# Kernel optimization log

Measured on AMD Instinct MI355X. Metric: run time of the kernel, lower is better.

## Reference

```python
import jax, jax.numpy as jnp
import numpy as np


def setup_inputs() -> dict:
    key = jax.random.key(0)
    k1, k2 = jax.random.split(key)
    X = jax.random.normal(k1, (8192, 3), dtype=jnp.float32)
    Y = jax.random.normal(k2, (8192, 3), dtype=jnp.float32)
    return {"X": X, "Y": Y}


def reference(X, Y):
    # Pairwise L2 distances: torch.norm(x - y) for every (x, y) pair.
    # d[i, j] = ||X[i] - Y[j]||_2, shape [N, M]
    diff = X[:, None, :] - Y[None, :, :]          # [N, M, D]
    d = jnp.sqrt(jnp.sum(diff * diff, axis=-1))   # [N, M]
    hd_xy = jnp.max(jnp.min(d, axis=1))           # max over x of min over y
    hd_yx = jnp.max(jnp.min(d, axis=0))           # max over y of min over x
    return jnp.maximum(hd_xy, hd_yx)
```

## Files before the change

kernel.cpp:

```cpp
#include <hip/hip_runtime.h>
#include <math.h>


typedef float v2f __attribute__((ext_vector_type(2)));

constexpr int NPTS = 8192;
constexpr int T = 256;
constexpr int R = 4;
constexpr int ROWS_PB = T * R;
constexpr int RG = NPTS / ROWS_PB;
constexpr int CG = 64;
constexpr int COLS = NPTS / CG;

__global__ __launch_bounds__(T) void pair_partial_kernel(
        const float* __restrict__ X, const float* __restrict__ Y,
        float* __restrict__ partial, float* __restrict__ out) {
    int b = blockIdx.x;
    if (b == 0 && threadIdx.x == 0) out[0] = 0.f;
    int dir = b / (RG * CG);
    int rem = b - dir * (RG * CG);
    int rg = rem / CG;
    int cg = rem - rg * CG;
    const float* A = dir ? Y : X;
    const float* B = dir ? X : Y;

    int t = threadIdx.x;
    int r0 = rg * ROWS_PB + t;

    float ax[R], ay[R], az[R];
#pragma unroll
    for (int k = 0; k < R; ++k) {
        int row = r0 + k * T;
        ax[k] = A[row * 3 + 0];
        ay[k] = A[row * 3 + 1];
        az[k] = A[row * 3 + 2];
    }

    __shared__ float4 Bs[COLS];
    for (int i = t; i < COLS; i += T) {
        int j = cg * COLS + i;
        float bx = B[j * 3 + 0], by = B[j * 3 + 1], bz = B[j * 3 + 2];
        Bs[i] = make_float4(bx, by, bz, -0.5f * fmaf(bx, bx, fmaf(by, by, bz * bz)));
    }

    v2f ax2[R / 2], ay2[R / 2], az2[R / 2], na2[R / 2], mt2[R / 2];
#pragma unroll
    for (int q = 0; q < R / 2; ++q) {
        ax2[q] = (v2f){ax[2 * q], ax[2 * q + 1]};
        ay2[q] = (v2f){ay[2 * q], ay[2 * q + 1]};
        az2[q] = (v2f){az[2 * q], az[2 * q + 1]};
        na2[q] = ax2[q] * ax2[q] + ay2[q] * ay2[q] + az2[q] * az2[q];
        mt2[q] = (v2f){-__builtin_inff(), -__builtin_inff()};
    }
    __syncthreads();

#pragma unroll 4
    for (int j = 0; j < COLS; ++j) {
        float4 p = Bs[j];
        v2f px = (v2f){p.x, p.x};
        v2f py = (v2f){p.y, p.y};
        v2f pz = (v2f){p.z, p.z};
        v2f pw = (v2f){p.w, p.w};
#pragma unroll
        for (int q = 0; q < R / 2; ++q) {
            v2f tt = az2[q] * pz + pw;
            tt = ay2[q] * py + tt;
            tt = ax2[q] * px + tt;
            mt2[q].x = fmaxf(mt2[q].x, tt.x);
            mt2[q].y = fmaxf(mt2[q].y, tt.y);
        }
    }

    float* op = partial + (size_t)(dir * CG + cg) * NPTS + rg * ROWS_PB + t;
#pragma unroll
    for (int q = 0; q < R / 2; ++q) {
        op[(2 * q) * T]     = fmaf(-2.f, mt2[q].x, na2[q].x);
        op[(2 * q + 1) * T] = fmaf(-2.f, mt2[q].y, na2[q].y);
    }
}

__global__ __launch_bounds__(T) void reduce_final_kernel(
        const float* __restrict__ partial, float* __restrict__ out) {
    int rid = blockIdx.x * T + threadIdx.x;
    int dir = rid >> 13;
    int row = rid & (NPTS - 1);
    const float* p = partial + (size_t)dir * CG * NPTS + row;

    float m[8];
#pragma unroll
    for (int k = 0; k < 8; ++k) m[k] = __builtin_inff();
#pragma unroll
    for (int cg = 0; cg < CG; ++cg)
        m[cg & 7] = fminf(m[cg & 7], p[(size_t)cg * NPTS]);
#pragma unroll
    for (int k = 0; k < 4; ++k) m[k] = fminf(m[k], m[k + 4]);
    float mm = fminf(fminf(m[0], m[1]), fminf(m[2], m[3]));
    float d = sqrtf(fmaxf(mm, 0.f));

    for (int o = 32; o > 0; o >>= 1) d = fmaxf(d, __shfl_down(d, o));
    __shared__ float wm[T / 64];
    if ((threadIdx.x & 63) == 0) wm[threadIdx.x >> 6] = d;
    __syncthreads();
    if (threadIdx.x == 0) {
        float bm = wm[0];
        for (int w = 1; w < T / 64; ++w) bm = fmaxf(bm, wm[w]);
        atomicMax((unsigned*)out, __float_as_uint(bm));
    }
}


constexpr int SEG_J = 512;
constexpr int SEGS = NPTS / SEG_J;

__global__ void init_min_kernel(unsigned* wsmin, int n) {
    int i = blockIdx.x * blockDim.x + threadIdx.x;
    if (i < n) wsmin[i] = 0x7F800000u;
}

__global__ __launch_bounds__(T) void pair_min_kernel(
        const float* __restrict__ X, const float* __restrict__ Y,
        unsigned* __restrict__ minXY, unsigned* __restrict__ minYX) {
    constexpr int RPB = T * 8;
    constexpr int BLOCKS_PER_DIR = (NPTS / RPB) * SEGS;
    int b = blockIdx.x;
    int dir = b / BLOCKS_PER_DIR;
    int rem = b - dir * BLOCKS_PER_DIR;
    int rg = rem / SEGS;
    int seg = rem - rg * SEGS;
    const float* A = dir ? Y : X;
    const float* B = dir ? X : Y;
    unsigned* omin = dir ? minYX : minXY;

    __shared__ float Bs[SEG_J * 3];
    int t = threadIdx.x;
    const float* Bseg = B + seg * SEG_J * 3;
    for (int i = t; i < SEG_J * 3; i += T) Bs[i] = Bseg[i];

    int r0 = rg * RPB + t;
    float ax[8], ay[8], az[8], m[8];
#pragma unroll
    for (int r = 0; r < 8; ++r) {
        int row = r0 + r * T;
        ax[r] = A[row * 3 + 0];
        ay[r] = A[row * 3 + 1];
        az[r] = A[row * 3 + 2];
        m[r] = __builtin_inff();
    }
    __syncthreads();

#pragma unroll 2
    for (int j = 0; j < SEG_J; ++j) {
        float bx = Bs[3 * j + 0], by = Bs[3 * j + 1], bz = Bs[3 * j + 2];
#pragma unroll
        for (int r = 0; r < 8; ++r) {
            float dx = ax[r] - bx, dy = ay[r] - by, dz = az[r] - bz;
            m[r] = fminf(m[r], fmaf(dx, dx, fmaf(dy, dy, dz * dz)));
        }
    }
#pragma unroll
    for (int r = 0; r < 8; ++r)
        atomicMin(&omin[r0 + r * T], __float_as_uint(m[r]));
}

__global__ __launch_bounds__(T) void finalize_min_kernel(
        const unsigned* __restrict__ wsmin, float* __restrict__ out, int n) {
    int t = threadIdx.x;
    float mx = 0.f;
    for (int i = t; i < n; i += T) mx = fmaxf(mx, __uint_as_float(wsmin[i]));
    for (int o = 32; o > 0; o >>= 1) mx = fmaxf(mx, __shfl_down(mx, o));
    __shared__ float wmax[T / 64];
    if ((t & 63) == 0) wmax[t >> 6] = mx;
    __syncthreads();
    if (t == 0) {
        float mm = wmax[0];
        for (int w = 1; w < T / 64; ++w) mm = fmaxf(mm, wmax[w]);
        out[0] = sqrtf(mm);
    }
}

extern "C" void kernel_launch(void* const* d_in, const int* in_sizes, int n_in,
                              void* d_out, int out_size, void* d_ws, size_t ws_size,
                              hipStream_t stream) {
    const float* X = (const float*)d_in[0];
    const float* Y = (const float*)d_in[1];
    float* out = (float*)d_out;

    const size_t need = (size_t)(2 * CG * NPTS) * sizeof(float);

    if (ws_size >= need) {
        float* partial = (float*)d_ws;
        pair_partial_kernel<<<2 * RG * CG, T, 0, stream>>>(X, Y, partial, out);
        reduce_final_kernel<<<2 * NPTS / T, T, 0, stream>>>(partial, out);
    } else if (ws_size >= 2 * NPTS * sizeof(unsigned)) {
        unsigned* wsmin = (unsigned*)d_ws;
        init_min_kernel<<<(2 * NPTS + T - 1) / T, T, 0, stream>>>(wsmin, 2 * NPTS);
        pair_min_kernel<<<2 * (NPTS / (T * 8)) * SEGS, T, 0, stream>>>(
            X, Y, wsmin, wsmin + NPTS);
        finalize_min_kernel<<<1, T, 0, stream>>>(wsmin, out, 2 * NPTS);
    }
}
```

Before: 29.78 us.

## Halve column groups and finish reduction with last-block atomic counter

```diff
diff --git a/kernel.cpp b/kernel.cpp
--- a/kernel.cpp
+++ b/kernel.cpp
@@ -9,14 +9,17 @@
 constexpr int R = 4;
 constexpr int ROWS_PB = T * R;
 constexpr int RG = NPTS / ROWS_PB;
-constexpr int CG = 64;
+constexpr int CG = 32;
 constexpr int COLS = NPTS / CG;
+
+constexpr int RT = 64;
+constexpr int RBLK = 2 * NPTS / RT;
 
 __global__ __launch_bounds__(T) void pair_partial_kernel(
         const float* __restrict__ X, const float* __restrict__ Y,
-        float* __restrict__ partial, float* __restrict__ out) {
+        float* __restrict__ partial, unsigned* __restrict__ counter) {
     int b = blockIdx.x;
-    if (b == 0 && threadIdx.x == 0) out[0] = 0.f;
+    if (b == 0 && threadIdx.x == 0) *counter = 0u;
     int dir = b / (RG * CG);
     int rem = b - dir * (RG * CG);
     int rg = rem / CG;
@@ -27,13 +30,14 @@
     int t = threadIdx.x;
     int r0 = rg * ROWS_PB + t;
 
-    float ax[R], ay[R], az[R];
-#pragma unroll
-    for (int k = 0; k < R; ++k) {
-        int row = r0 + k * T;
-        ax[k] = A[row * 3 + 0];
-        ay[k] = A[row * 3 + 1];
-        az[k] = A[row * 3 + 2];
+    v2f ax2[R / 2], ay2[R / 2], az2[R / 2], na2[R / 2], mt2[R / 2];
+#pragma unroll
+    for (int q = 0; q < R / 2; ++q) {
+        int ra = r0 + (2 * q) * T;
+        int rb = r0 + (2 * q + 1) * T;
+        ax2[q] = (v2f){A[ra * 3 + 0], A[rb * 3 + 0]};
+        ay2[q] = (v2f){A[ra * 3 + 1], A[rb * 3 + 1]};
+        az2[q] = (v2f){A[ra * 3 + 2], A[rb * 3 + 2]};
     }
 
     __shared__ float4 Bs[COLS];
@@ -43,18 +47,14 @@
         Bs[i] = make_float4(bx, by, bz, -0.5f * fmaf(bx, bx, fmaf(by, by, bz * bz)));
     }
 
-    v2f ax2[R / 2], ay2[R / 2], az2[R / 2], na2[R / 2], mt2[R / 2];
 #pragma unroll
     for (int q = 0; q < R / 2; ++q) {
-        ax2[q] = (v2f){ax[2 * q], ax[2 * q + 1]};
-        ay2[q] = (v2f){ay[2 * q], ay[2 * q + 1]};
-        az2[q] = (v2f){az[2 * q], az[2 * q + 1]};
         na2[q] = ax2[q] * ax2[q] + ay2[q] * ay2[q] + az2[q] * az2[q];
         mt2[q] = (v2f){-__builtin_inff(), -__builtin_inff()};
     }
     __syncthreads();
 
-#pragma unroll 4
+#pragma unroll 8
     for (int j = 0; j < COLS; ++j) {
         float4 p = Bs[j];
         v2f px = (v2f){p.x, p.x};
@@ -66,8 +66,7 @@
             v2f tt = az2[q] * pz + pw;
             tt = ay2[q] * py + tt;
             tt = ax2[q] * px + tt;
-            mt2[q].x = fmaxf(mt2[q].x, tt.x);
-            mt2[q].y = fmaxf(mt2[q].y, tt.y);
+            mt2[q] = __builtin_elementwise_max(mt2[q], tt);
         }
     }
 
@@ -79,9 +78,10 @@
     }
 }
 
-__global__ __launch_bounds__(T) void reduce_final_kernel(
-        const float* __restrict__ partial, float* __restrict__ out) {
-    int rid = blockIdx.x * T + threadIdx.x;
+__global__ __launch_bounds__(RT) void reduce_final_kernel(
+        const float* __restrict__ partial, float* __restrict__ blockmax,
+        unsigned* __restrict__ counter, float* __restrict__ out) {
+    int rid = blockIdx.x * RT + threadIdx.x;
     int dir = rid >> 13;
     int row = rid & (NPTS - 1);
     const float* p = partial + (size_t)dir * CG * NPTS + row;
@@ -94,34 +94,46 @@
         m[cg & 7] = fminf(m[cg & 7], p[(size_t)cg * NPTS]);
 #pragma unroll
     for (int k = 0; k < 4; ++k) m[k] = fminf(m[k], m[k + 4]);
-    float mm = fminf(fminf(m[0], m[1]), fminf(m[2], m[3]));
-    float d = sqrtf(fmaxf(mm, 0.f));
-
-    for (int o = 32; o > 0; o >>= 1) d = fmaxf(d, __shfl_down(d, o));
-    __shared__ float wm[T / 64];
-    if ((threadIdx.x & 63) == 0) wm[threadIdx.x >> 6] = d;
-    __syncthreads();
-    if (threadIdx.x == 0) {
-        float bm = wm[0];
-        for (int w = 1; w < T / 64; ++w) bm = fmaxf(bm, wm[w]);
-        atomicMax((unsigned*)out, __float_as_uint(bm));
-    }
-}
-
-
-constexpr int SEG_J = 512;
-constexpr int SEGS = NPTS / SEG_J;
+    float mm = fmaxf(fminf(fminf(m[0], m[1]), fminf(m[2], m[3])), 0.f);
+
+#pragma unroll
+    for (int o = 32; o > 0; o >>= 1) mm = fmaxf(mm, __shfl_xor(mm, o));
+    if (threadIdx.x == 0)
+        __hip_atomic_store(&blockmax[blockIdx.x], mm, __ATOMIC_RELEASE,
+                           __HIP_MEMORY_SCOPE_AGENT);
+
+    __shared__ unsigned is_last;
+    if (threadIdx.x == 0)
+        is_last = (__hip_atomic_fetch_add(counter, 1u, __ATOMIC_ACQ_REL,
+                                          __HIP_MEMORY_SCOPE_AGENT) == RBLK - 1);
+    __syncthreads();
+    if (!is_last) return;
+
+    float bm = 0.f;
+#pragma unroll
+    for (int k = 0; k < RBLK / RT; ++k) {
+        float v = __hip_atomic_load(&blockmax[k * RT + threadIdx.x],
+                                    __ATOMIC_ACQUIRE, __HIP_MEMORY_SCOPE_AGENT);
+        bm = fmaxf(bm, v);
+    }
+#pragma unroll
+    for (int o = 32; o > 0; o >>= 1) bm = fmaxf(bm, __shfl_xor(bm, o));
+    if (threadIdx.x == 0) out[0] = sqrtf(bm);
+}
+
 
 __global__ void init_min_kernel(unsigned* wsmin, int n) {
     int i = blockIdx.x * blockDim.x + threadIdx.x;
     if (i < n) wsmin[i] = 0x7F800000u;
 }
 
-__global__ __launch_bounds__(T) void pair_min_kernel(
+__global__ __launch_bounds__(256) void pair_min_kernel(
         const float* __restrict__ X, const float* __restrict__ Y,
         unsigned* __restrict__ minXY, unsigned* __restrict__ minYX) {
-    constexpr int RPB = T * 8;
-    constexpr int BLOCKS_PER_DIR = (NPTS / RPB) * SEGS;
+    constexpr int SEG_J = 512;
+    constexpr int SEGS = NPTS / SEG_J;
+    constexpr int RPB8 = 256 * 8;
+    constexpr int BLOCKS_PER_DIR = (NPTS / RPB8) * SEGS;
     int b = blockIdx.x;
     int dir = b / BLOCKS_PER_DIR;
     int rem = b - dir * BLOCKS_PER_DIR;
@@ -134,13 +146,13 @@
     __shared__ float Bs[SEG_J * 3];
     int t = threadIdx.x;
     const float* Bseg = B + seg * SEG_J * 3;
-    for (int i = t; i < SEG_J * 3; i += T) Bs[i] = Bseg[i];
-
-    int r0 = rg * RPB + t;
+    for (int i = t; i < SEG_J * 3; i += 256) Bs[i] = Bseg[i];
+
+    int r0 = rg * RPB8 + t;
     float ax[8], ay[8], az[8], m[8];
 #pragma unroll
     for (int r = 0; r < 8; ++r) {
-        int row = r0 + r * T;
+        int row = r0 + r * 256;
         ax[r] = A[row * 3 + 0];
         ay[r] = A[row * 3 + 1];
         az[r] = A[row * 3 + 2];
@@ -159,21 +171,20 @@
     }
 #pragma unroll
     for (int r = 0; r < 8; ++r)
-        atomicMin(&omin[r0 + r * T], __float_as_uint(m[r]));
-}
-
-__global__ __launch_bounds__(T) void finalize_min_kernel(
+        atomicMin(&omin[r0 + r * 256], __float_as_uint(m[r]));
+}
+
+__global__ __launch_bounds__(256) void finalize_min_kernel(
         const unsigned* __restrict__ wsmin, float* __restrict__ out, int n) {
     int t = threadIdx.x;
     float mx = 0.f;
-    for (int i = t; i < n; i += T) mx = fmaxf(mx, __uint_as_float(wsmin[i]));
+    for (int i = t; i < n; i += 256) mx = fmaxf(mx, __uint_as_float(wsmin[i]));
     for (int o = 32; o > 0; o >>= 1) mx = fmaxf(mx, __shfl_down(mx, o));
-    __shared__ float wmax[T / 64];
+    __shared__ float wmax[4];
     if ((t & 63) == 0) wmax[t >> 6] = mx;
     __syncthreads();
     if (t == 0) {
-        float mm = wmax[0];
-        for (int w = 1; w < T / 64; ++w) mm = fmaxf(mm, wmax[w]);
+        float mm = fmaxf(fmaxf(wmax[0], wmax[1]), fmaxf(wmax[2], wmax[3]));
         out[0] = sqrtf(mm);
     }
 }
@@ -185,17 +196,20 @@
     const float* Y = (const float*)d_in[1];
     float* out = (float*)d_out;
 
-    const size_t need = (size_t)(2 * CG * NPTS) * sizeof(float);
+    const size_t partial_elems = (size_t)2 * CG * NPTS;
+    const size_t need = (partial_elems + RBLK + 1) * sizeof(float);
 
     if (ws_size >= need) {
         float* partial = (float*)d_ws;
-        pair_partial_kernel<<<2 * RG * CG, T, 0, stream>>>(X, Y, partial, out);
-        reduce_final_kernel<<<2 * NPTS / T, T, 0, stream>>>(partial, out);
+        float* blockmax = partial + partial_elems;
+        unsigned* counter = (unsigned*)(blockmax + RBLK);
+        pair_partial_kernel<<<2 * RG * CG, T, 0, stream>>>(X, Y, partial, counter);
+        reduce_final_kernel<<<RBLK, RT, 0, stream>>>(partial, blockmax, counter, out);
     } else if (ws_size >= 2 * NPTS * sizeof(unsigned)) {
         unsigned* wsmin = (unsigned*)d_ws;
-        init_min_kernel<<<(2 * NPTS + T - 1) / T, T, 0, stream>>>(wsmin, 2 * NPTS);
-        pair_min_kernel<<<2 * (NPTS / (T * 8)) * SEGS, T, 0, stream>>>(
+        init_min_kernel<<<(2 * NPTS + 255) / 256, 256, 0, stream>>>(wsmin, 2 * NPTS);
+        pair_min_kernel<<<2 * (NPTS / (256 * 8)) * (NPTS / 512), 256, 0, stream>>>(
             X, Y, wsmin, wsmin + NPTS);
-        finalize_min_kernel<<<1, T, 0, stream>>>(wsmin, out, 2 * NPTS);
-    }
-}
+        finalize_min_kernel<<<1, 256, 0, stream>>>(wsmin, out, 2 * NPTS);
+    }
+}
```

New measurement: 28.49 us. 1.05x faster.
